# Performance work log

Hardware: AMD Instinct MI355X
Metric: run time of the kernel (lower is better)

## Reference

```python
import jax, jax.numpy as jnp
import numpy as np


def _gru(x, h, Wih, Whh, bih, bhh):
    # torch.nn.GRUCell math. x:(1,in), h:(1,H), Wih:(3H,in), Whh:(3H,H)
    gi = x @ Wih.T + bih
    gh = h @ Whh.T + bhh
    i_r, i_z, i_n = jnp.split(gi, 3, axis=-1)
    h_r, h_z, h_n = jnp.split(gh, 3, axis=-1)
    r = jax.nn.sigmoid(i_r + h_r)
    z = jax.nn.sigmoid(i_z + h_z)
    n = jnp.tanh(i_n + r * h_n)
    return (1.0 - z) * n + z * h


def _combine(S, Wa, ba, va):
    # SelfAttention.combine: additive attention over the stack axis.
    # S:(k,1,H), Wa:(H,A), ba:(A,), va:(A,)
    e = jnp.tanh(S @ Wa + ba) @ va          # (k,1) energies
    w = jax.nn.softmax(e, axis=0)            # softmax over stacked hidden states
    return jnp.sum(w[..., None] * S, axis=0)  # (1,H)


def setup_inputs() -> dict:
    key = jax.random.key(0)
    ks = jax.random.split(key, 20)
    T, F, H, A, L = 16384, 2048, 16, 64, 6
    G = 3 * H
    s = 0.1  # weight scale for numerical sanity
    return {
        "batch": jax.random.normal(ks[0], (T, 1, F), jnp.float32),
        "h0": jax.random.normal(ks[1], (L, 1, H), jnp.float32),
        "W_ih0": jax.random.normal(ks[2], (G, F), jnp.float32) * s,
        "W_hh0": jax.random.normal(ks[3], (G, H), jnp.float32) * s,
        "b_ih0": jax.random.normal(ks[4], (G,), jnp.float32) * s,
        "b_hh0": jax.random.normal(ks[5], (G,), jnp.float32) * s,
        "W_ih": jax.random.normal(ks[6], (L - 1, G, H), jnp.float32) * s,
        "W_hh": jax.random.normal(ks[7], (L - 1, G, H), jnp.float32) * s,
        "b_ih": jax.random.normal(ks[8], (L - 1, G), jnp.float32) * s,
        "b_hh": jax.random.normal(ks[9], (L - 1, G), jnp.float32) * s,
        "Wa": jax.random.normal(ks[10], (L, H, A), jnp.float32) * s,
        "ba": jax.random.normal(ks[11], (L, A), jnp.float32) * s,
        "va": jax.random.normal(ks[12], (L, A), jnp.float32) * s,
        "fc1_w": jax.random.normal(ks[13], (32, H), jnp.float32) * s,
        "fc1_b": jax.random.normal(ks[14], (32,), jnp.float32) * s,
        "fc2_w": jax.random.normal(ks[15], (1, 32), jnp.float32) * s,
        "fc2_b": jax.random.normal(ks[16], (1,), jnp.float32) * s,
    }


def reference(batch, h0, W_ih0, W_hh0, b_ih0, b_hh0, W_ih, W_hh, b_ih, b_hh,
              Wa, ba, va, fc1_w, fc1_b, fc2_w, fc2_b):
    L = Wa.shape[0]

    def step(h_s, x):
        # h_s: (L,1,H) carried hidden states, x: (1,F) current token
        inp = x.reshape(1, -1)
        new = []
        for l in range(L):
            if l == 0:
                inp = _gru(inp, h_s[0], W_ih0, W_hh0, b_ih0, b_hh0)
            else:
                inp = _gru(inp, h_s[l], W_ih[l - 1], W_hh[l - 1], b_ih[l - 1], b_hh[l - 1])
            new.append(inp)
        newS = jnp.stack(new)  # (L,1,H)
        # layer i attends over hidden states of layers i..L-1 (feedback combine)
        h_next = jnp.stack([_combine(newS[i:], Wa[i], ba[i], va[i]) for i in range(L)])
        top = h_next[-1].reshape(-1)  # (H,); dropout is identity in eval mode
        out = (top @ fc1_w.T + fc1_b) @ fc2_w.T + fc2_b  # (1,)
        return h_next, out

    _, outs = jax.lax.scan(step, h0, batch)
    return outs  # (T,1)
```

## Files before the change

### kernel.cpp

```cpp
#include <hip/hip_runtime.h>
#include <cstdint>
#include <cstddef>


#define TT 16384
#define FF 2048
#define HH 16
#define LL 6
#define GG 48
#define CHUNK 64
#define LOG2E 1.44269504088896340736f

__device__ float g_gi0p[(TT + CHUNK) * 64];

__device__ __forceinline__ float exp2_(float x) { return __builtin_amdgcn_exp2f(x); }
__device__ __forceinline__ float rcp_(float x) { return __builtin_amdgcn_rcpf(x); }
__device__ __forceinline__ float sig_n(float s) { return rcp_(1.f + exp2_(s)); }
__device__ __forceinline__ float tanh_p(float s) { return fmaf(-2.f, rcp_(exp2_(s) + 1.f), 1.f); }

#define MEMBAR() __asm__ __volatile__("" ::: "memory")

__device__ __forceinline__ float rdlane(float v, int l) {
  union { float f; int i; } a, b;
  a.f = v; b.i = __builtin_amdgcn_readlane(a.i, l); return b.f;
}
template <int CTRL>
__device__ __forceinline__ float dppf(float v) {
  union { float f; int i; } a, b;
  a.f = v; b.i = __builtin_amdgcn_mov_dpp(a.i, CTRL, 0xF, 0xF, true); return b.f;
}
template <int Q>
__device__ __forceinline__ float qbcast(float v) { return dppf<Q | (Q << 2) | (Q << 4) | (Q << 6)>(v); }

__device__ __forceinline__ float rowsum16(float v) {
  v += dppf<0xB1>(v);
  v += dppf<0x4E>(v);
  v += dppf<0x141>(v);
  v += dppf<0x140>(v);
  return v;
}
__device__ __forceinline__ float dot16r(const float (&w)[16], const float (&h)[16]) {
  float s0 = w[0] * h[0], s1 = w[1] * h[1], s2 = w[2] * h[2], s3 = w[3] * h[3];
#pragma unroll
  for (int k = 4; k < 16; k += 4) {
    s0 = fmaf(w[k], h[k], s0);       s1 = fmaf(w[k + 1], h[k + 1], s1);
    s2 = fmaf(w[k + 2], h[k + 2], s2); s3 = fmaf(w[k + 3], h[k + 3], s3);
  }
  return (s0 + s1) + (s2 + s3);
}
__device__ __forceinline__ float dot16i(const float (&w)[16], const float (&h)[16], float init) {
  float s0 = fmaf(w[0], h[0], init), s1 = w[1] * h[1], s2 = w[2] * h[2], s3 = w[3] * h[3];
#pragma unroll
  for (int k = 4; k < 16; k += 4) {
    s0 = fmaf(w[k], h[k], s0);       s1 = fmaf(w[k + 1], h[k + 1], s1);
    s2 = fmaf(w[k + 2], h[k + 2], s2); s3 = fmaf(w[k + 3], h[k + 3], s3);
  }
  return (s0 + s1) + (s2 + s3);
}

__device__ __forceinline__ int ldAcq(int* f) {
  return __hip_atomic_load(f, __ATOMIC_ACQUIRE, __HIP_MEMORY_SCOPE_WORKGROUP);
}
__device__ __forceinline__ void pollGE(int* f, int target) {
  while (ldAcq(f) < target) {}
}
__device__ __forceinline__ void waitFlag(int* f, int& cache, int need) {
  if (cache < need) { do { cache = ldAcq(f); } while (cache < need); }
}
__device__ __forceinline__ void sigRel(int* f, int v) {
  __hip_atomic_store(f, v, __ATOMIC_RELAXED, __HIP_MEMORY_SCOPE_WORKGROUP);
}

__device__ __forceinline__ void combBlock(const float4 A0, const float4 A1, const float4 A2,
                                          const float4 A3, float nsv,
                                          const float (&Wa)[16], float ba, float va,
                                          const float (&Wh)[16],
                                          float& S, float& ha, float& Pa) {
  float nr[16] = {A0.x, A0.y, A0.z, A0.w, A1.x, A1.y, A1.z, A1.w,
                  A2.x, A2.y, A2.z, A2.w, A3.x, A3.y, A3.z, A3.w};
  float u = dot16i(Wa, nr, ba);
  float P = dot16r(Wh, nr);
  float pe = va * tanh_p(u);
  float r = rowsum16(pe);
  float e = (rdlane(r, 0) + rdlane(r, 16)) + (rdlane(r, 32) + rdlane(r, 48));
  float w = exp2_(e);
  S += w; ha = fmaf(w, nsv, ha); Pa = fmaf(w, P, Pa);
}

__global__ __launch_bounds__(256) void gi0_gemm(const float* __restrict__ X,
                                                const float* __restrict__ W,
                                                const float* __restrict__ bias) {
  __shared__ float xs[64][132];
  __shared__ float ws[48][132];
  const int tid = threadIdx.x;
  const int t0 = blockIdx.x * 64;
  const int tg = tid & 15;
  const int tt = tid >> 4;
  float acc[4][3];
#pragma unroll
  for (int u = 0; u < 4; ++u)
#pragma unroll
    for (int v = 0; v < 3; ++v) acc[u][v] = 0.f;

  for (int k0 = 0; k0 < FF; k0 += 128) {
#pragma unroll
    for (int i = 0; i < 32; ++i) {
      int e = tid + 256 * i; int r = e >> 7, c = e & 127;
      xs[r][c] = X[(size_t)(t0 + r) * FF + k0 + c];
    }
#pragma unroll
    for (int i = 0; i < 24; ++i) {
      int e = tid + 256 * i; int r = e >> 7, c = e & 127;
      ws[r][c] = W[(size_t)r * FF + k0 + c];
    }
    __syncthreads();
#pragma unroll 8
    for (int c = 0; c < 128; ++c) {
      float x0 = xs[tt][c], x1 = xs[tt + 16][c], x2 = xs[tt + 32][c], x3 = xs[tt + 48][c];
      float w0 = ws[tg][c], w1 = ws[tg + 16][c], w2 = ws[tg + 32][c];
      acc[0][0] += x0 * w0; acc[0][1] += x0 * w1; acc[0][2] += x0 * w2;
      acc[1][0] += x1 * w0; acc[1][1] += x1 * w1; acc[1][2] += x1 * w2;
      acc[2][0] += x2 * w0; acc[2][1] += x2 * w1; acc[2][2] += x2 * w2;
      acc[3][0] += x3 * w0; acc[3][1] += x3 * w1; acc[3][2] += x3 * w2;
    }
    __syncthreads();
  }
  const float gsc3[3] = {-LOG2E, -LOG2E, 2.f * LOG2E};
#pragma unroll
  for (int u = 0; u < 4; ++u)
#pragma unroll
    for (int v = 0; v < 3; ++v)
      g_gi0p[(size_t)(t0 + tt + 16 * u) * 64 + tg * 4 + v] =
          (acc[u][v] + bias[tg + 16 * v]) * gsc3[v];
}

__global__ __launch_bounds__(512, 1) void fbrnn_scan(
    const float* __restrict__ h0,
    const float* __restrict__ Whh0, const float* __restrict__ bhh0,
    const float* __restrict__ Wih, const float* __restrict__ Whh,
    const float* __restrict__ bih, const float* __restrict__ bhh,
    const float* __restrict__ Wa, const float* __restrict__ ba,
    const float* __restrict__ va,
    const float* __restrict__ fc1w, const float* __restrict__ fc1b,
    const float* __restrict__ fc2w, const float* __restrict__ fc2b,
    float* __restrict__ out) {
  __shared__ __align__(16) float nsS[2][LL * HH];
  __shared__ __align__(16) float4 recS[5 * 64];
  __shared__ __align__(16) float4 partS[4 * 64];
  __shared__ __align__(16) float nsOut[256 * HH];
  __shared__ __align__(16) float chunkS[2][CHUNK * 64];
  __shared__ int flagNs;
  __shared__ int flagChunk;
  __shared__ int flagOut;
  __shared__ int gen5[2];

  const int tid = threadIdx.x;
  const int wv = tid >> 6;
  const int lane = tid & 63;
  const int qg = lane & 3;
  const int kk = lane >> 2;
  const int gate = (qg < 3 ? qg : 2);
  const int G = gate * 16 + kk;
  const float gsc = (gate == 2) ? 2.f * LOG2E : -LOG2E;

  const bool isChain = (wv == 0);
  const bool isStream = (wv == 4);
  const bool isFc = (wv == 6);
  const bool isIdle = (wv == 1);
  const int hRow = (wv == 6) ? 0 : (wv == 2) ? 1 : -1;
  const int pRow = (wv == 3) ? 2 : (wv == 7) ? 3 : (wv == 5) ? 4 : -1;
  const int pSlot = (wv == 6) ? 0 : (wv == 2) ? 2 : -1;

  float WBih[5][16];
  float WB5[16];  float bhh5R = 0.f;
  float Wa0R[16], Wh0R[16], Wa1R[16], Wh1R[16];
  float ba0R = 0.f, va0R = 0.f, bb0 = 0.f;
  float ba1R = 0.f, va1R = 0.f, bb1 = 0.f;
  float WaP[16], WhP[16];
  float baP = 0.f, vaP = 0.f, bhhP = 0.f;
  float WaH[16], WhH[16];
  float baH = 0.f, vaH = 0.f;
  float fc1R[16];
  float fb1 = 0.f, fw2 = 0.f, fb2 = 0.f;

  if (isChain) {
#pragma unroll
    for (int l = 0; l < 5; ++l)
#pragma unroll
      for (int k = 0; k < 16; ++k) WBih[l][k] = Wih[((l * GG) + G) * 16 + k] * gsc;
#pragma unroll
    for (int k = 0; k < 16; ++k) WB5[k] = Whh[(4 * GG + G) * 16 + k] * gsc;
    bhh5R = (bhh[4 * GG + G] + bih[4 * GG + G]) * gsc;
#pragma unroll
    for (int k = 0; k < 16; ++k) {
      Wa0R[k] = Wa[(0 * 16 + k) * 64 + lane] * (2.f * LOG2E);
      Wa1R[k] = Wa[(1 * 16 + k) * 64 + lane] * (2.f * LOG2E);
      Wh0R[k] = Whh0[G * 16 + k] * gsc;
      Wh1R[k] = Whh[(0 * GG + G) * 16 + k] * gsc;
    }
    ba0R = ba[0 * 64 + lane] * (2.f * LOG2E); va0R = va[0 * 64 + lane] * LOG2E;
    ba1R = ba[1 * 64 + lane] * (2.f * LOG2E); va1R = va[1 * 64 + lane] * LOG2E;
    bb0 = bhh0[G] * gsc;
    bb1 = (bhh[0 * GG + G] + bih[0 * GG + G]) * gsc;
  }
  if (pRow >= 0) {
#pragma unroll
    for (int k = 0; k < 16; ++k) WaP[k] = Wa[(pRow * 16 + k) * 64 + lane] * (2.f * LOG2E);
    baP = ba[pRow * 64 + lane] * (2.f * LOG2E);
    vaP = va[pRow * 64 + lane] * LOG2E;
    const float* ws = Whh + ((pRow - 1) * GG + G) * 16;
#pragma unroll
    for (int k = 0; k < 16; ++k) WhP[k] = ws[k] * gsc;
    bhhP = (bhh[(pRow - 1) * GG + G] + bih[(pRow - 1) * GG + G]) * gsc;
  }
  if (hRow >= 0) {
#pragma unroll
    for (int k = 0; k < 16; ++k) WaH[k] = Wa[(hRow * 16 + k) * 64 + lane] * (2.f * LOG2E);
    baH = ba[hRow * 64 + lane] * (2.f * LOG2E);
    vaH = va[hRow * 64 + lane] * LOG2E;
    const float* ws = (hRow == 0) ? (Whh0 + G * 16) : (Whh + ((hRow - 1) * GG + G) * 16);
#pragma unroll
    for (int k = 0; k < 16; ++k) WhH[k] = ws[k] * gsc;
  }
  if (isFc) {
    const int m = lane & 31;
#pragma unroll
    for (int k = 0; k < 16; ++k) fc1R[k] = fc1w[m * 16 + k];
    fb1 = fc1b[m]; fw2 = fc2w[m]; fb2 = fc2b[0];
  }

  if (tid == 0) { flagNs = 0; flagChunk = 1; flagOut = 0; gen5[0] = 0; gen5[1] = 0; }

  float hv5m = 0.f, gh5reg = 0.f;
  float gh0n = 0.f, hv0m = 0.f, gh1n = 0.f, hv1m = 0.f;
  if (isChain) {
    float hr[16];
#pragma unroll
    for (int k = 0; k < 16; ++k) hr[k] = h0[5 * 16 + k];
    hv5m = h0[5 * 16 + kk] - 1.f;
    gh5reg = dot16i(WB5, hr, bhh5R);
#pragma unroll
    for (int k = 0; k < 16; ++k) hr[k] = h0[0 * 16 + k];
    hv0m = h0[0 * 16 + kk] - 1.f;
    gh0n = dot16i(Wh0R, hr, bb0);
#pragma unroll
    for (int k = 0; k < 16; ++k) hr[k] = h0[1 * 16 + k];
    hv1m = h0[1 * 16 + kk] - 1.f;
    gh1n = dot16i(Wh1R, hr, bb1);
  } else if (pRow >= 0) {
    float hr[16];
#pragma unroll
    for (int k = 0; k < 16; ++k) hr[k] = h0[pRow * 16 + k];
    float4 rr;
    rr.x = dot16i(WhP, hr, bhhP);
    rr.y = h0[pRow * 16 + kk] - 1.f;
    rr.z = __int_as_float(0);
    rr.w = 0.f;
    recS[pRow * 64 + lane] = rr;
  }
  if (isStream) {
    const float4* src = (const float4*)g_gi0p;
    float4* dst = (float4*)(&chunkS[0][0]);
#pragma unroll
    for (int q = 0; q < 16; ++q) dst[q * 64 + lane] = src[q * 64 + lane];
  }
  if (pSlot >= 0) partS[pSlot * 64 + lane] = make_float4(0.f, 0.f, 0.f, __int_as_float(0));
  __syncthreads();

  if (isIdle) return;

#define EBLOCK(J, WaX, baX, vaX, WhX, Sx, hax, Pax) do {                          \
    waitFlag(&flagNs, fcache, t * 8 + (J) + 1);                                   \
    const float4* np_ = (const float4*)&nsS[nb][(J) * 16];                        \
    float4 A0_ = np_[0], A1_ = np_[1], A2_ = np_[2], A3_ = np_[3];                \
    float nsv_ = nsS[nb][(J) * 16 + kk];                                          \
    combBlock(A0_, A1_, A2_, A3_, nsv_, WaX, baX, vaX, WhX, Sx, hax, Pax);        \
  } while (0)

#define TAILFIN(ROW, Sv, hav, Pav) do {                                           \
    float4 A0, A1, A2, A3; float nsv5;                                            \
    for (;;) {                                                                    \
      int g5 = ldAcq(&gen5[nb]);                                                  \
      MEMBAR();                                                                   \
      const float4* np = (const float4*)&nsS[nb][5 * 16];                         \
      A0 = np[0]; A1 = np[1]; A2 = np[2]; A3 = np[3];                             \
      nsv5 = nsS[nb][5 * 16 + kk];                                                \
      MEMBAR();                                                                   \
      if (g5 >= tgt) break;                                                       \
    }                                                                             \
    combBlock(A0, A1, A2, A3, nsv5, WaP, baP, vaP, WhP, Sv, hav, Pav);            \
    const float inv_ = rcp_(Sv);                                                  \
    float4 rr_; rr_.x = fmaf(Pav, inv_, bhhP); rr_.y = fmaf(hav, inv_, -1.f);     \
    rr_.z = __int_as_float(tgt); rr_.w = 0.f;                                     \
    recS[(ROW) * 64 + lane] = rr_;                                                \
  } while (0)

  if (isStream) {
#pragma unroll 1
    for (int c = 1; c < 256; ++c) {
      if (c >= 2) pollGE(&flagNs, ((c - 1) * 64 - 1) * 8 + 1);
      const float4* src = (const float4*)(g_gi0p + ((size_t)c << 12));
      float4* dst = (float4*)(&chunkS[c & 1][0]);
#pragma unroll
      for (int q = 0; q < 16; ++q) dst[q * 64 + lane] = src[q * 64 + lane];
      MEMBAR();
      sigRel(&flagChunk, c + 1);
    }
    return;
  }

  if (isFc) {
    int fcache = 0;
#pragma unroll 1
    for (int t = 0; t < TT; ++t) {
      const int nb = t & 1;
      float Sh = 0.f, hah = 0.f, Pah = 0.f;
      EBLOCK(0, WaH, baH, vaH, WhH, Sh, hah, Pah);
      EBLOCK(1, WaH, baH, vaH, WhH, Sh, hah, Pah);
      EBLOCK(2, WaH, baH, vaH, WhH, Sh, hah, Pah);
      MEMBAR();
      partS[0 * 64 + lane] = make_float4(Sh, hah, Pah, __int_as_float(t + 1));
      MEMBAR();
      waitFlag(&flagNs, fcache, t * 8 + 6);
      const float4* np = (const float4*)(nsOut + (t & 255) * 16);
      float4 a0 = np[0], a1 = np[1], a2 = np[2], a3 = np[3];
      float nr[16] = {a0.x, a0.y, a0.z, a0.w, a1.x, a1.y, a1.z, a1.w,
                      a2.x, a2.y, a2.z, a2.w, a3.x, a3.y, a3.z, a3.w};
      float y = dot16i(fc1R, nr, fb1);
      float p = rowsum16(y * fw2);
      float o = rdlane(p, 0) + rdlane(p, 16) + fb2;
      if (lane == 0) out[t] = o;
      MEMBAR();
      sigRel(&flagOut, t + 1);
    }
    return;
  }

  if (!isChain) {
    int fcache = 0;
    if (wv == 2) {
#pragma unroll 1
      for (int t = 0; t < TT; ++t) {
        const int nb = t & 1;
        float Sh = 0.f, hah = 0.f, Pah = 0.f;
        EBLOCK(1, WaH, baH, vaH, WhH, Sh, hah, Pah);
        EBLOCK(2, WaH, baH, vaH, WhH, Sh, hah, Pah);
        MEMBAR();
        partS[2 * 64 + lane] = make_float4(Sh, hah, Pah, __int_as_float(t + 1));
        MEMBAR();
      }
    } else if (wv == 3) {
#pragma unroll 1
      for (int t = 0; t < TT; ++t) {
        const int nb = t & 1;
        const int tgt = t + 1;
        float S = 0.f, ha = 0.f, Pa = 0.f;
        EBLOCK(2, WaP, baP, vaP, WhP, S, ha, Pa);
        EBLOCK(3, WaP, baP, vaP, WhP, S, ha, Pa);
        EBLOCK(4, WaP, baP, vaP, WhP, S, ha, Pa);
        TAILFIN(2, S, ha, Pa);
      }
    } else if (wv == 7) {
#pragma unroll 1
      for (int t = 0; t < TT; ++t) {
        const int nb = t & 1;
        const int tgt = t + 1;
        float S = 0.f, ha = 0.f, Pa = 0.f;
        EBLOCK(3, WaP, baP, vaP, WhP, S, ha, Pa);
        EBLOCK(4, WaP, baP, vaP, WhP, S, ha, Pa);
        TAILFIN(3, S, ha, Pa);
      }
    } else {
#pragma unroll 1
      for (int t = 0; t < TT; ++t) {
        const int nb = t & 1;
        const int tgt = t + 1;
        float S = 0.f, ha = 0.f, Pa = 0.f;
        EBLOCK(4, WaP, baP, vaP, WhP, S, ha, Pa);
        TAILFIN(4, S, ha, Pa);
      }
    }
    return;
  }

  float gnext = chunkS[0][lane];
  float ns_sg[16];
#pragma unroll 1
  for (int t = 0; t < TT; ++t) {
    const int wb = t & 1;

    float ghv[6], hvm1[6];
    ghv[0] = gh0n; hvm1[0] = hv0m;
    ghv[1] = gh1n; hvm1[1] = hv1m;
    ghv[5] = gh5reg; hvm1[5] = hv5m;
    float4 r2, r3, r4;
    float gpre = 0.f;
    float gi0v = gnext;
    float ns = 0.f;
    float S0a = 0.f, ha0a = 0.f, Pa0a = 0.f;
    float S1a = 0.f, ha1a = 0.f, Pa1a = 0.f;
#pragma unroll
    for (int l = 0; l < 6; ++l) {
      if (l == 2) {
        if (!((__float_as_int(r2.z) >= t) & (__float_as_int(r3.z) >= t) &
              (__float_as_int(r4.z) >= t))) {
          do {
            MEMBAR();
            r2 = recS[2 * 64 + lane]; r3 = recS[3 * 64 + lane]; r4 = recS[4 * 64 + lane];
            MEMBAR();
          } while (!((__float_as_int(r2.z) >= t) & (__float_as_int(r3.z) >= t) &
                     (__float_as_int(r4.z) >= t)));
        }
        ghv[2] = r2.x; hvm1[2] = r2.y;
        ghv[3] = r3.x; hvm1[3] = r3.y;
        ghv[4] = r4.x; hvm1[4] = r4.y;
      }
      const float gh_g = ghv[l];
      const float s = (l == 0) ? (gi0v + gh_g) : dot16i(WBih[l - 1], ns_sg, gh_g);
      const float sg = sig_n(s);
      const float smg = s - gh_g;
      const float sr = qbcast<0>(sg);
      const float sz = qbcast<1>(sg);
      const float nb2 = fmaf(2.f, sz, -2.f);
      const float apb = fmaf(sz, hvm1[l], 1.f);
      const float E = exp2_(fmaf(sr, gh_g, smg));
      const float R = rcp_(E + 1.f);
      ns = fmaf(nb2, R, apb);
      if (qg == 2) {
        nsS[wb][l * 16 + kk] = ns;
        if (l == 5) nsOut[(t & 255) * 16 + kk] = ns;
      }
      MEMBAR();
      if (l == 5 && lane == 0) { sigRel(&gen5[wb], t + 1); sigRel(&flagNs, t * 8 + 6); }
#pragma unroll
      for (int k = 0; k < 16; ++k) ns_sg[k] = rdlane(ns, 4 * k + 2);
      if (l < 5 && lane == 0) sigRel(&flagNs, t * 8 + l + 1);
      if (l == 0) {
        if ((t & 63) == 63) {
          const int cn = (t + 1) >> 6;
          if (cn < 256) pollGE(&flagChunk, cn + 1);
        }
        if ((t & 63) == 32) pollGE(&flagOut, t - 64);
        gpre = chunkS[((t + 1) >> 6) & 1][((t + 1) & 63) * 64 + lane];
        MEMBAR();
        r2 = recS[2 * 64 + lane]; r3 = recS[3 * 64 + lane]; r4 = recS[4 * 64 + lane];
        MEMBAR();
      }
      if (l == 3 || l == 4) {
        const float nsq = qbcast<2>(ns);
        float uj0 = dot16i(Wa0R, ns_sg, ba0R);
        float uj1 = dot16i(Wa1R, ns_sg, ba1R);
        float Pj0 = dot16r(Wh0R, ns_sg);
        float Pj1 = dot16r(Wh1R, ns_sg);
        float pj0 = va0R * tanh_p(uj0);
        float pj1 = va1R * tanh_p(uj1);
        float rj0 = rowsum16(pj0);
        float rj1 = rowsum16(pj1);
        float ej0 = (rdlane(rj0, 0) + rdlane(rj0, 16)) + (rdlane(rj0, 32) + rdlane(rj0, 48));
        float ej1 = (rdlane(rj1, 0) + rdlane(rj1, 16)) + (rdlane(rj1, 32) + rdlane(rj1, 48));
        float wj0_ = exp2_(ej0), wj1_ = exp2_(ej1);
        S0a += wj0_; ha0a = fmaf(wj0_, nsq, ha0a); Pa0a = fmaf(wj0_, Pj0, Pa0a);
        S1a += wj1_; ha1a = fmaf(wj1_, nsq, ha1a); Pa1a = fmaf(wj1_, Pj1, Pa1a);
      }
    }
    MEMBAR();
    float4 q0 = partS[0 * 64 + lane], q2 = partS[2 * 64 + lane];
    MEMBAR();
    const float hv5n = qbcast<2>(ns);
    gh5reg = dot16i(WB5, ns_sg, bhh5R);
    float u0 = dot16i(Wa0R, ns_sg, ba0R);
    float u1 = dot16i(Wa1R, ns_sg, ba1R);
    float P0 = dot16r(Wh0R, ns_sg);
    float P1 = dot16r(Wh1R, ns_sg);
    float pe0 = va0R * tanh_p(u0);
    float pe1 = va1R * tanh_p(u1);
    float rs0 = rowsum16(pe0);
    float rs1 = rowsum16(pe1);
    float e0 = (rdlane(rs0, 0) + rdlane(rs0, 16)) + (rdlane(rs0, 32) + rdlane(rs0, 48));
    float e1 = (rdlane(rs1, 0) + rdlane(rs1, 16)) + (rdlane(rs1, 32) + rdlane(rs1, 48));
    float wj0 = exp2_(e0), wj1 = exp2_(e1);
    const int tp = t + 1;
    if (!((__float_as_int(q0.w) >= tp) & (__float_as_int(q2.w) >= tp))) {
      do {
        MEMBAR();
        q0 = partS[0 * 64 + lane]; q2 = partS[2 * 64 + lane];
        MEMBAR();
      } while (!((__float_as_int(q0.w) >= tp) & (__float_as_int(q2.w) >= tp)));
    }
    float S0 = q0.x + S0a + wj0;
    float hT0 = q0.y + ha0a + wj0 * hv5n;
    float PT0 = q0.z + Pa0a + wj0 * P0;
    float S1 = q2.x + S1a + wj1;
    float hT1 = q2.y + ha1a + wj1 * hv5n;
    float PT1 = q2.z + Pa1a + wj1 * P1;
    const float inv0 = rcp_(S0);
    const float inv1 = rcp_(S1);
    gh0n = fmaf(PT0, inv0, bb0); hv0m = fmaf(hT0, inv0, -1.f);
    gh1n = fmaf(PT1, inv1, bb1); hv1m = fmaf(hT1, inv1, -1.f);
    hv5m = hv5n - 1.f;
    gnext = gpre;
  }
}

extern "C" void kernel_launch(void* const* d_in, const int* in_sizes, int n_in,
                              void* d_out, int out_size, void* d_ws, size_t ws_size,
                              hipStream_t stream) {
  const float* batch = (const float*)d_in[0];
  const float* h0    = (const float*)d_in[1];
  const float* Wih0  = (const float*)d_in[2];
  const float* Whh0  = (const float*)d_in[3];
  const float* bih0  = (const float*)d_in[4];
  const float* bhh0  = (const float*)d_in[5];
  const float* Wih   = (const float*)d_in[6];
  const float* Whh   = (const float*)d_in[7];
  const float* bih   = (const float*)d_in[8];
  const float* bhh   = (const float*)d_in[9];
  const float* Wa    = (const float*)d_in[10];
  const float* ba    = (const float*)d_in[11];
  const float* va    = (const float*)d_in[12];
  const float* fc1w  = (const float*)d_in[13];
  const float* fc1b  = (const float*)d_in[14];
  const float* fc2w  = (const float*)d_in[15];
  const float* fc2b  = (const float*)d_in[16];
  float* out = (float*)d_out;
  (void)in_sizes; (void)n_in; (void)out_size; (void)d_ws; (void)ws_size;

  gi0_gemm<<<TT / 64, 256, 0, stream>>>(batch, Wih0, bih0);
  fbrnn_scan<<<1, 512, 0, stream>>>(h0, Whh0, bhh0, Wih, Whh, bih, bhh,
                                    Wa, ba, va, fc1w, fc1b, fc2w, fc2b, out);
}
```

Baseline: 27.54 ms.

## Offload layer 0/1/5 attention finalisation from chain wave to dedicated wavefronts

The chain wavefront no longer computes the attention combine for rows 0 and 1 or the layer-5 recurrent projection. Those move to the previously idle wave 1, which waits on the layer-5 state and gathers six partial sums from other waves. Partial-sum work is redistributed across waves 2, 3, 5, 6 and 7, and results are published through recS slots that the chain polls. This shortens the serial critical path per step, at the cost of an extra cross-wave handoff through shared memory that the chain must wait on before layer 0.

```diff
diff --git a/kernel.cpp b/kernel.cpp
--- a/kernel.cpp
+++ b/kernel.cpp
@@ -145,8 +145,8 @@
     const float* __restrict__ fc2w, const float* __restrict__ fc2b,
     float* __restrict__ out) {
   __shared__ __align__(16) float nsS[2][LL * HH];
-  __shared__ __align__(16) float4 recS[5 * 64];
-  __shared__ __align__(16) float4 partS[4 * 64];
+  __shared__ __align__(16) float4 recS[6 * 64];
+  __shared__ __align__(16) float4 partS[6 * 64];
   __shared__ __align__(16) float nsOut[256 * HH];
   __shared__ __align__(16) float chunkS[2][CHUNK * 64];
   __shared__ int flagNs;
@@ -164,99 +164,95 @@
   const float gsc = (gate == 2) ? 2.f * LOG2E : -LOG2E;
 
   const bool isChain = (wv == 0);
+  const bool isFin = (wv == 1);
   const bool isStream = (wv == 4);
   const bool isFc = (wv == 6);
-  const bool isIdle = (wv == 1);
-  const int hRow = (wv == 6) ? 0 : (wv == 2) ? 1 : -1;
-  const int pRow = (wv == 3) ? 2 : (wv == 7) ? 3 : (wv == 5) ? 4 : -1;
-  const int pSlot = (wv == 6) ? 0 : (wv == 2) ? 2 : -1;
+  const int tailRow = (wv == 3) ? 2 : (wv == 7) ? 3 : (wv == 5) ? 4 : -1;
 
   float WBih[5][16];
   float WB5[16];  float bhh5R = 0.f;
   float Wa0R[16], Wh0R[16], Wa1R[16], Wh1R[16];
   float ba0R = 0.f, va0R = 0.f, bb0 = 0.f;
   float ba1R = 0.f, va1R = 0.f, bb1 = 0.f;
-  float WaP[16], WhP[16];
-  float baP = 0.f, vaP = 0.f, bhhP = 0.f;
-  float WaH[16], WhH[16];
-  float baH = 0.f, vaH = 0.f;
-  float fc1R[16];
-  float fb1 = 0.f, fw2 = 0.f, fb2 = 0.f;
+  float WaA[16], WhA[16]; float baA = 0.f, vaA = 0.f;
+  float WaB[16], WhB[16]; float baB = 0.f, vaB = 0.f;
+  float WaT[16], WhT[16]; float baT = 0.f, vaT = 0.f, bhT = 0.f;
+  float fc1R[16]; float fb1 = 0.f, fw2 = 0.f, fb2 = 0.f;
+
+#define LOADROW(R, WaX, baX, vaX, WhX) do {                                      \
+    _Pragma("unroll") for (int k = 0; k < 16; ++k)                               \
+      WaX[k] = Wa[((R) * 16 + k) * 64 + lane] * (2.f * LOG2E);                   \
+    baX = ba[(R) * 64 + lane] * (2.f * LOG2E);                                   \
+    vaX = va[(R) * 64 + lane] * LOG2E;                                           \
+    { const float* ws_ = ((R) == 0) ? (Whh0 + G * 16)                            \
+                                    : (Whh + (((R) - 1) * GG + G) * 16);         \
+      _Pragma("unroll") for (int k = 0; k < 16; ++k) WhX[k] = ws_[k] * gsc; }    \
+  } while (0)
+#define LOADBH(R, bhX) do {                                                      \
+    bhX = (((R) == 0) ? bhh0[G]                                                  \
+                      : (bhh[((R) - 1) * GG + G] + bih[((R) - 1) * GG + G])) *   \
+          gsc;                                                                   \
+  } while (0)
 
   if (isChain) {
 #pragma unroll
     for (int l = 0; l < 5; ++l)
 #pragma unroll
       for (int k = 0; k < 16; ++k) WBih[l][k] = Wih[((l * GG) + G) * 16 + k] * gsc;
+  } else if (isFin) {
 #pragma unroll
     for (int k = 0; k < 16; ++k) WB5[k] = Whh[(4 * GG + G) * 16 + k] * gsc;
     bhh5R = (bhh[4 * GG + G] + bih[4 * GG + G]) * gsc;
-#pragma unroll
-    for (int k = 0; k < 16; ++k) {
-      Wa0R[k] = Wa[(0 * 16 + k) * 64 + lane] * (2.f * LOG2E);
-      Wa1R[k] = Wa[(1 * 16 + k) * 64 + lane] * (2.f * LOG2E);
-      Wh0R[k] = Whh0[G * 16 + k] * gsc;
-      Wh1R[k] = Whh[(0 * GG + G) * 16 + k] * gsc;
-    }
-    ba0R = ba[0 * 64 + lane] * (2.f * LOG2E); va0R = va[0 * 64 + lane] * LOG2E;
-    ba1R = ba[1 * 64 + lane] * (2.f * LOG2E); va1R = va[1 * 64 + lane] * LOG2E;
-    bb0 = bhh0[G] * gsc;
-    bb1 = (bhh[0 * GG + G] + bih[0 * GG + G]) * gsc;
-  }
-  if (pRow >= 0) {
-#pragma unroll
-    for (int k = 0; k < 16; ++k) WaP[k] = Wa[(pRow * 16 + k) * 64 + lane] * (2.f * LOG2E);
-    baP = ba[pRow * 64 + lane] * (2.f * LOG2E);
-    vaP = va[pRow * 64 + lane] * LOG2E;
-    const float* ws = Whh + ((pRow - 1) * GG + G) * 16;
-#pragma unroll
-    for (int k = 0; k < 16; ++k) WhP[k] = ws[k] * gsc;
-    bhhP = (bhh[(pRow - 1) * GG + G] + bih[(pRow - 1) * GG + G]) * gsc;
-  }
-  if (hRow >= 0) {
-#pragma unroll
-    for (int k = 0; k < 16; ++k) WaH[k] = Wa[(hRow * 16 + k) * 64 + lane] * (2.f * LOG2E);
-    baH = ba[hRow * 64 + lane] * (2.f * LOG2E);
-    vaH = va[hRow * 64 + lane] * LOG2E;
-    const float* ws = (hRow == 0) ? (Whh0 + G * 16) : (Whh + ((hRow - 1) * GG + G) * 16);
-#pragma unroll
-    for (int k = 0; k < 16; ++k) WhH[k] = ws[k] * gsc;
-  }
-  if (isFc) {
+    LOADROW(0, Wa0R, ba0R, va0R, Wh0R); LOADBH(0, bb0);
+    LOADROW(1, Wa1R, ba1R, va1R, Wh1R); LOADBH(1, bb1);
+  } else if (isFc) {
+    LOADROW(0, WaA, baA, vaA, WhA);
     const int m = lane & 31;
 #pragma unroll
     for (int k = 0; k < 16; ++k) fc1R[k] = fc1w[m * 16 + k];
     fb1 = fc1b[m]; fw2 = fc2w[m]; fb2 = fc2b[0];
+  } else if (wv == 2) {
+    LOADROW(1, WaA, baA, vaA, WhA);
+    LOADROW(0, WaB, baB, vaB, WhB);
+  } else if (wv == 3) {
+    LOADROW(2, WaT, baT, vaT, WhT); LOADBH(2, bhT);
+  } else if (wv == 5) {
+    LOADROW(1, WaA, baA, vaA, WhA);
+    LOADROW(4, WaT, baT, vaT, WhT); LOADBH(4, bhT);
+  } else if (wv == 7) {
+    LOADROW(1, WaA, baA, vaA, WhA);
+    LOADROW(3, WaT, baT, vaT, WhT); LOADBH(3, bhT);
   }
 
   if (tid == 0) { flagNs = 0; flagChunk = 1; flagOut = 0; gen5[0] = 0; gen5[1] = 0; }
 
-  float hv5m = 0.f, gh5reg = 0.f;
-  float gh0n = 0.f, hv0m = 0.f, gh1n = 0.f, hv1m = 0.f;
-  if (isChain) {
+  if (isFin) {
     float hr[16];
 #pragma unroll
+    for (int k = 0; k < 16; ++k) hr[k] = h0[0 * 16 + k];
+    float4 r0i; r0i.x = dot16i(Wh0R, hr, bb0); r0i.y = h0[0 * 16 + kk] - 1.f;
+    r0i.z = __int_as_float(0); r0i.w = 0.f;
+    recS[0 * 64 + lane] = r0i;
+#pragma unroll
+    for (int k = 0; k < 16; ++k) hr[k] = h0[1 * 16 + k];
+    float4 r1i; r1i.x = dot16i(Wh1R, hr, bb1); r1i.y = h0[1 * 16 + kk] - 1.f;
+    r1i.z = __int_as_float(0); r1i.w = 0.f;
+    recS[1 * 64 + lane] = r1i;
+#pragma unroll
     for (int k = 0; k < 16; ++k) hr[k] = h0[5 * 16 + k];
-    hv5m = h0[5 * 16 + kk] - 1.f;
-    gh5reg = dot16i(WB5, hr, bhh5R);
-#pragma unroll
-    for (int k = 0; k < 16; ++k) hr[k] = h0[0 * 16 + k];
-    hv0m = h0[0 * 16 + kk] - 1.f;
-    gh0n = dot16i(Wh0R, hr, bb0);
-#pragma unroll
-    for (int k = 0; k < 16; ++k) hr[k] = h0[1 * 16 + k];
-    hv1m = h0[1 * 16 + kk] - 1.f;
-    gh1n = dot16i(Wh1R, hr, bb1);
-  } else if (pRow >= 0) {
+    float4 r5i; r5i.x = dot16i(WB5, hr, bhh5R); r5i.y = h0[5 * 16 + kk] - 1.f;
+    r5i.z = __int_as_float(0); r5i.w = 0.f;
+    recS[5 * 64 + lane] = r5i;
+  } else if (tailRow >= 0) {
     float hr[16];
 #pragma unroll
-    for (int k = 0; k < 16; ++k) hr[k] = h0[pRow * 16 + k];
+    for (int k = 0; k < 16; ++k) hr[k] = h0[tailRow * 16 + k];
     float4 rr;
-    rr.x = dot16i(WhP, hr, bhhP);
-    rr.y = h0[pRow * 16 + kk] - 1.f;
+    rr.x = dot16i(WhT, hr, bhT);
+    rr.y = h0[tailRow * 16 + kk] - 1.f;
     rr.z = __int_as_float(0);
     rr.w = 0.f;
-    recS[pRow * 64 + lane] = rr;
+    recS[tailRow * 64 + lane] = rr;
   }
   if (isStream) {
     const float4* src = (const float4*)g_gi0p;
@@ -264,10 +260,12 @@
 #pragma unroll
     for (int q = 0; q < 16; ++q) dst[q * 64 + lane] = src[q * 64 + lane];
   }
-  if (pSlot >= 0) partS[pSlot * 64 + lane] = make_float4(0.f, 0.f, 0.f, __int_as_float(0));
+  if (isFc) {
+#pragma unroll
+    for (int s = 0; s < 6; ++s)
+      partS[s * 64 + lane] = make_float4(0.f, 0.f, 0.f, __int_as_float(0));
+  }
   __syncthreads();
-
-  if (isIdle) return;
 
 #define EBLOCK(J, WaX, baX, vaX, WhX, Sx, hax, Pax) do {                          \
     waitFlag(&flagNs, fcache, t * 8 + (J) + 1);                                   \
@@ -275,6 +273,12 @@
     float4 A0_ = np_[0], A1_ = np_[1], A2_ = np_[2], A3_ = np_[3];                \
     float nsv_ = nsS[nb][(J) * 16 + kk];                                          \
     combBlock(A0_, A1_, A2_, A3_, nsv_, WaX, baX, vaX, WhX, Sx, hax, Pax);        \
+  } while (0)
+
+#define POSTP(SLOT, Sx, hax, Pax) do {                                            \
+    MEMBAR();                                                                     \
+    partS[(SLOT) * 64 + lane] = make_float4(Sx, hax, Pax, __int_as_float(t + 1)); \
+    MEMBAR();                                                                     \
   } while (0)
 
 #define TAILFIN(ROW, Sv, hav, Pav) do {                                           \
@@ -288,9 +292,9 @@
       MEMBAR();                                                                   \
       if (g5 >= tgt) break;                                                       \
     }                                                                             \
-    combBlock(A0, A1, A2, A3, nsv5, WaP, baP, vaP, WhP, Sv, hav, Pav);            \
+    combBlock(A0, A1, A2, A3, nsv5, WaT, baT, vaT, WhT, Sv, hav, Pav);            \
     const float inv_ = rcp_(Sv);                                                  \
-    float4 rr_; rr_.x = fmaf(Pav, inv_, bhhP); rr_.y = fmaf(hav, inv_, -1.f);     \
+    float4 rr_; rr_.x = fmaf(Pav, inv_, bhT); rr_.y = fmaf(hav, inv_, -1.f);      \
     rr_.z = __int_as_float(tgt); rr_.w = 0.f;                                     \
     recS[(ROW) * 64 + lane] = rr_;                                                \
   } while (0)
@@ -309,24 +313,88 @@
     return;
   }
 
+  if (isFin) {
+#pragma unroll 1
+    for (int t = 0; t < TT; ++t) {
+      const int nb = t & 1;
+      const int tgt = t + 1;
+      float4 A0, A1, A2, A3; float nsv5;
+      for (;;) {
+        int g5 = ldAcq(&gen5[nb]);
+        MEMBAR();
+        const float4* np = (const float4*)&nsS[nb][5 * 16];
+        A0 = np[0]; A1 = np[1]; A2 = np[2]; A3 = np[3];
+        nsv5 = nsS[nb][5 * 16 + kk];
+        MEMBAR();
+        if (g5 >= tgt) break;
+      }
+      float nr[16] = {A0.x, A0.y, A0.z, A0.w, A1.x, A1.y, A1.z, A1.w,
+                      A2.x, A2.y, A2.z, A2.w, A3.x, A3.y, A3.z, A3.w};
+      float u0 = dot16i(Wa0R, nr, ba0R);
+      float u1 = dot16i(Wa1R, nr, ba1R);
+      float P0 = dot16r(Wh0R, nr);
+      float P1 = dot16r(Wh1R, nr);
+      float g5d = dot16i(WB5, nr, bhh5R);
+      float pe0 = va0R * tanh_p(u0);
+      float pe1 = va1R * tanh_p(u1);
+      float rs0 = rowsum16(pe0);
+      float rs1 = rowsum16(pe1);
+      float e0 = (rdlane(rs0, 0) + rdlane(rs0, 16)) + (rdlane(rs0, 32) + rdlane(rs0, 48));
+      float e1 = (rdlane(rs1, 0) + rdlane(rs1, 16)) + (rdlane(rs1, 32) + rdlane(rs1, 48));
+      float wj0 = exp2_(e0), wj1 = exp2_(e1);
+      float4 q0, q1, q2, q3, q4, q5;
+      for (;;) {
+        MEMBAR();
+        q0 = partS[0 * 64 + lane]; q1 = partS[1 * 64 + lane]; q2 = partS[2 * 64 + lane];
+        q3 = partS[3 * 64 + lane]; q4 = partS[4 * 64 + lane]; q5 = partS[5 * 64 + lane];
+        MEMBAR();
+        int ok = (__float_as_int(q0.w) >= tgt) & (__float_as_int(q1.w) >= tgt) &
+                 (__float_as_int(q2.w) >= tgt) & (__float_as_int(q3.w) >= tgt) &
+                 (__float_as_int(q4.w) >= tgt) & (__float_as_int(q5.w) >= tgt);
+        if (ok) break;
+      }
+      float S0 = q0.x + q1.x + q2.x + wj0;
+      float hT0 = q0.y + q1.y + q2.y + wj0 * nsv5;
+      float PT0 = q0.z + q1.z + q2.z + wj0 * P0;
+      float S1 = q3.x + q4.x + q5.x + wj1;
+      float hT1 = q3.y + q4.y + q5.y + wj1 * nsv5;
+      float PT1 = q3.z + q4.z + q5.z + wj1 * P1;
+      const float inv0 = rcp_(S0);
+      const float inv1 = rcp_(S1);
+      float4 w0r; w0r.x = fmaf(PT0, inv0, bb0); w0r.y = fmaf(hT0, inv0, -1.f);
+      w0r.z = __int_as_float(tgt); w0r.w = 0.f;
+      float4 w1r; w1r.x = fmaf(PT1, inv1, bb1); w1r.y = fmaf(hT1, inv1, -1.f);
+      w1r.z = __int_as_float(tgt); w1r.w = 0.f;
+      float4 w5r; w5r.x = g5d; w5r.y = nsv5 - 1.f;
+      w5r.z = __int_as_float(tgt); w5r.w = 0.f;
+      MEMBAR();
+      recS[0 * 64 + lane] = w0r;
+      recS[1 * 64 + lane] = w1r;
+      recS[5 * 64 + lane] = w5r;
+      MEMBAR();
+    }
+    return;
+  }
+
   if (isFc) {
     int fcache = 0;
 #pragma unroll 1
     for (int t = 0; t < TT; ++t) {
       const int nb = t & 1;
-      float Sh = 0.f, hah = 0.f, Pah = 0.f;
-      EBLOCK(0, WaH, baH, vaH, WhH, Sh, hah, Pah);
-      EBLOCK(1, WaH, baH, vaH, WhH, Sh, hah, Pah);
-      EBLOCK(2, WaH, baH, vaH, WhH, Sh, hah, Pah);
-      MEMBAR();
-      partS[0 * 64 + lane] = make_float4(Sh, hah, Pah, __int_as_float(t + 1));
-      MEMBAR();
+      float S = 0.f, ha = 0.f, Pa = 0.f;
+      EBLOCK(0, WaA, baA, vaA, WhA, S, ha, Pa);
+      EBLOCK(1, WaA, baA, vaA, WhA, S, ha, Pa);
+      EBLOCK(2, WaA, baA, vaA, WhA, S, ha, Pa);
+      POSTP(0, S, ha, Pa);
+      S = 0.f; ha = 0.f; Pa = 0.f;
+      EBLOCK(4, WaA, baA, vaA, WhA, S, ha, Pa);
+      POSTP(2, S, ha, Pa);
       waitFlag(&flagNs, fcache, t * 8 + 6);
       const float4* np = (const float4*)(nsOut + (t & 255) * 16);
       float4 a0 = np[0], a1 = np[1], a2 = np[2], a3 = np[3];
-      float nr[16] = {a0.x, a0.y, a0.z, a0.w, a1.x, a1.y, a1.z, a1.w,
-                      a2.x, a2.y, a2.z, a2.w, a3.x, a3.y, a3.z, a3.w};
-      float y = dot16i(fc1R, nr, fb1);
+      float nrf[16] = {a0.x, a0.y, a0.z, a0.w, a1.x, a1.y, a1.z, a1.w,
+                       a2.x, a2.y, a2.z, a2.w, a3.x, a3.y, a3.z, a3.w};
+      float y = dot16i(fc1R, nrf, fb1);
       float p = rowsum16(y * fw2);
       float o = rdlane(p, 0) + rdlane(p, 16) + fb2;
       if (lane == 0) out[t] = o;
@@ -342,23 +410,25 @@
 #pragma unroll 1
       for (int t = 0; t < TT; ++t) {
         const int nb = t & 1;
-        float Sh = 0.f, hah = 0.f, Pah = 0.f;
-        EBLOCK(1, WaH, baH, vaH, WhH, Sh, hah, Pah);
-        EBLOCK(2, WaH, baH, vaH, WhH, Sh, hah, Pah);
-        MEMBAR();
-        partS[2 * 64 + lane] = make_float4(Sh, hah, Pah, __int_as_float(t + 1));
-        MEMBAR();
-      }
-    } else if (wv == 3) {
+        float S = 0.f, ha = 0.f, Pa = 0.f;
+        EBLOCK(1, WaA, baA, vaA, WhA, S, ha, Pa);
+        EBLOCK(2, WaA, baA, vaA, WhA, S, ha, Pa);
+        POSTP(3, S, ha, Pa);
+        S = 0.f; ha = 0.f; Pa = 0.f;
+        EBLOCK(3, WaB, baB, vaB, WhB, S, ha, Pa);
+        POSTP(1, S, ha, Pa);
+      }
+    } else if (wv == 5) {
 #pragma unroll 1
       for (int t = 0; t < TT; ++t) {
         const int nb = t & 1;
         const int tgt = t + 1;
         float S = 0.f, ha = 0.f, Pa = 0.f;
-        EBLOCK(2, WaP, baP, vaP, WhP, S, ha, Pa);
-        EBLOCK(3, WaP, baP, vaP, WhP, S, ha, Pa);
-        EBLOCK(4, WaP, baP, vaP, WhP, S, ha, Pa);
-        TAILFIN(2, S, ha, Pa);
+        EBLOCK(3, WaA, baA, vaA, WhA, S, ha, Pa);
+        POSTP(4, S, ha, Pa);
+        S = 0.f; ha = 0.f; Pa = 0.f;
+        EBLOCK(4, WaT, baT, vaT, WhT, S, ha, Pa);
+        TAILFIN(4, S, ha, Pa);
       }
     } else if (wv == 7) {
 #pragma unroll 1
@@ -366,8 +436,11 @@
         const int nb = t & 1;
         const int tgt = t + 1;
         float S = 0.f, ha = 0.f, Pa = 0.f;
-        EBLOCK(3, WaP, baP, vaP, WhP, S, ha, Pa);
-        EBLOCK(4, WaP, baP, vaP, WhP, S, ha, Pa);
+        EBLOCK(3, WaT, baT, vaT, WhT, S, ha, Pa);
+        float Sb = 0.f, hab = 0.f, Pab = 0.f;
+        EBLOCK(4, WaA, baA, vaA, WhA, Sb, hab, Pab);
+        POSTP(5, Sb, hab, Pab);
+        EBLOCK(4, WaT, baT, vaT, WhT, S, ha, Pa);
         TAILFIN(3, S, ha, Pa);
       }
     } else {
@@ -376,8 +449,10 @@
         const int nb = t & 1;
         const int tgt = t + 1;
         float S = 0.f, ha = 0.f, Pa = 0.f;
-        EBLOCK(4, WaP, baP, vaP, WhP, S, ha, Pa);
-        TAILFIN(4, S, ha, Pa);
+        EBLOCK(2, WaT, baT, vaT, WhT, S, ha, Pa);
+        EBLOCK(3, WaT, baT, vaT, WhT, S, ha, Pa);
+        EBLOCK(4, WaT, baT, vaT, WhT, S, ha, Pa);
+        TAILFIN(2, S, ha, Pa);
       }
     }
     return;
@@ -389,31 +464,43 @@
   for (int t = 0; t < TT; ++t) {
     const int wb = t & 1;
 
+    if ((t & 63) == 63) {
+      const int cn = (t + 1) >> 6;
+      if (cn < 256) pollGE(&flagChunk, cn + 1);
+    }
+    if ((t & 63) == 32) pollGE(&flagOut, t - 64);
+    const float gpre = chunkS[((t + 1) >> 6) & 1][((t + 1) & 63) * 64 + lane];
+
+    float4 r0, r1;
+    for (;;) {
+      MEMBAR();
+      r0 = recS[0 * 64 + lane]; r1 = recS[1 * 64 + lane];
+      MEMBAR();
+      if ((__float_as_int(r0.z) >= t) & (__float_as_int(r1.z) >= t)) break;
+    }
     float ghv[6], hvm1[6];
-    ghv[0] = gh0n; hvm1[0] = hv0m;
-    ghv[1] = gh1n; hvm1[1] = hv1m;
-    ghv[5] = gh5reg; hvm1[5] = hv5m;
-    float4 r2, r3, r4;
-    float gpre = 0.f;
+    ghv[0] = r0.x; hvm1[0] = r0.y;
+    ghv[1] = r1.x; hvm1[1] = r1.y;
+    float4 r2, r3, r4, r5;
     float gi0v = gnext;
     float ns = 0.f;
-    float S0a = 0.f, ha0a = 0.f, Pa0a = 0.f;
-    float S1a = 0.f, ha1a = 0.f, Pa1a = 0.f;
 #pragma unroll
     for (int l = 0; l < 6; ++l) {
       if (l == 2) {
         if (!((__float_as_int(r2.z) >= t) & (__float_as_int(r3.z) >= t) &
-              (__float_as_int(r4.z) >= t))) {
+              (__float_as_int(r4.z) >= t) & (__float_as_int(r5.z) >= t))) {
           do {
             MEMBAR();
-            r2 = recS[2 * 64 + lane]; r3 = recS[3 * 64 + lane]; r4 = recS[4 * 64 + lane];
+            r2 = recS[2 * 64 + lane]; r3 = recS[3 * 64 + lane];
+            r4 = recS[4 * 64 + lane]; r5 = recS[5 * 64 + lane];
             MEMBAR();
           } while (!((__float_as_int(r2.z) >= t) & (__float_as_int(r3.z) >= t) &
-                     (__float_as_int(r4.z) >= t)));
+                     (__float_as_int(r4.z) >= t) & (__float_as_int(r5.z) >= t)));
         }
         ghv[2] = r2.x; hvm1[2] = r2.y;
         ghv[3] = r3.x; hvm1[3] = r3.y;
         ghv[4] = r4.x; hvm1[4] = r4.y;
+        ghv[5] = r5.x; hvm1[5] = r5.y;
       }
       const float gh_g = ghv[l];
       const float s = (l == 0) ? (gi0v + gh_g) : dot16i(WBih[l - 1], ns_sg, gh_g);
@@ -431,73 +518,20 @@
         if (l == 5) nsOut[(t & 255) * 16 + kk] = ns;
       }
       MEMBAR();
-      if (l == 5 && lane == 0) { sigRel(&gen5[wb], t + 1); sigRel(&flagNs, t * 8 + 6); }
-#pragma unroll
-      for (int k = 0; k < 16; ++k) ns_sg[k] = rdlane(ns, 4 * k + 2);
-      if (l < 5 && lane == 0) sigRel(&flagNs, t * 8 + l + 1);
+      if (l == 5) {
+        if (lane == 0) { sigRel(&gen5[wb], t + 1); sigRel(&flagNs, t * 8 + 6); }
+      } else {
+#pragma unroll
+        for (int k = 0; k < 16; ++k) ns_sg[k] = rdlane(ns, 4 * k + 2);
+        if (lane == 0) sigRel(&flagNs, t * 8 + l + 1);
+      }
       if (l == 0) {
-        if ((t & 63) == 63) {
-          const int cn = (t + 1) >> 6;
-          if (cn < 256) pollGE(&flagChunk, cn + 1);
-        }
-        if ((t & 63) == 32) pollGE(&flagOut, t - 64);
-        gpre = chunkS[((t + 1) >> 6) & 1][((t + 1) & 63) * 64 + lane];
         MEMBAR();
-        r2 = recS[2 * 64 + lane]; r3 = recS[3 * 64 + lane]; r4 = recS[4 * 64 + lane];
+        r2 = recS[2 * 64 + lane]; r3 = recS[3 * 64 + lane];
+        r4 = recS[4 * 64 + lane]; r5 = recS[5 * 64 + lane];
         MEMBAR();
       }
-      if (l == 3 || l == 4) {
-        const float nsq = qbcast<2>(ns);
-        float uj0 = dot16i(Wa0R, ns_sg, ba0R);
-        float uj1 = dot16i(Wa1R, ns_sg, ba1R);
-        float Pj0 = dot16r(Wh0R, ns_sg);
-        float Pj1 = dot16r(Wh1R, ns_sg);
-        float pj0 = va0R * tanh_p(uj0);
-        float pj1 = va1R * tanh_p(uj1);
-        float rj0 = rowsum16(pj0);
-        float rj1 = rowsum16(pj1);
-        float ej0 = (rdlane(rj0, 0) + rdlane(rj0, 16)) + (rdlane(rj0, 32) + rdlane(rj0, 48));
-        float ej1 = (rdlane(rj1, 0) + rdlane(rj1, 16)) + (rdlane(rj1, 32) + rdlane(rj1, 48));
-        float wj0_ = exp2_(ej0), wj1_ = exp2_(ej1);
-        S0a += wj0_; ha0a = fmaf(wj0_, nsq, ha0a); Pa0a = fmaf(wj0_, Pj0, Pa0a);
-        S1a += wj1_; ha1a = fmaf(wj1_, nsq, ha1a); Pa1a = fmaf(wj1_, Pj1, Pa1a);
-      }
-    }
-    MEMBAR();
-    float4 q0 = partS[0 * 64 + lane], q2 = partS[2 * 64 + lane];
-    MEMBAR();
-    const float hv5n = qbcast<2>(ns);
-    gh5reg = dot16i(WB5, ns_sg, bhh5R);
-    float u0 = dot16i(Wa0R, ns_sg, ba0R);
-    float u1 = dot16i(Wa1R, ns_sg, ba1R);
-    float P0 = dot16r(Wh0R, ns_sg);
-    float P1 = dot16r(Wh1R, ns_sg);
-    float pe0 = va0R * tanh_p(u0);
-    float pe1 = va1R * tanh_p(u1);
-    float rs0 = rowsum16(pe0);
-    float rs1 = rowsum16(pe1);
-    float e0 = (rdlane(rs0, 0) + rdlane(rs0, 16)) + (rdlane(rs0, 32) + rdlane(rs0, 48));
-    float e1 = (rdlane(rs1, 0) + rdlane(rs1, 16)) + (rdlane(rs1, 32) + rdlane(rs1, 48));
-    float wj0 = exp2_(e0), wj1 = exp2_(e1);
-    const int tp = t + 1;
-    if (!((__float_as_int(q0.w) >= tp) & (__float_as_int(q2.w) >= tp))) {
-      do {
-        MEMBAR();
-        q0 = partS[0 * 64 + lane]; q2 = partS[2 * 64 + lane];
-        MEMBAR();
-      } while (!((__float_as_int(q0.w) >= tp) & (__float_as_int(q2.w) >= tp)));
-    }
-    float S0 = q0.x + S0a + wj0;
-    float hT0 = q0.y + ha0a + wj0 * hv5n;
-    float PT0 = q0.z + Pa0a + wj0 * P0;
-    float S1 = q2.x + S1a + wj1;
-    float hT1 = q2.y + ha1a + wj1 * hv5n;
-    float PT1 = q2.z + Pa1a + wj1 * P1;
-    const float inv0 = rcp_(S0);
-    const float inv1 = rcp_(S1);
-    gh0n = fmaf(PT0, inv0, bb0); hv0m = fmaf(hT0, inv0, -1.f);
-    gh1n = fmaf(PT1, inv1, bb1); hv1m = fmaf(hT1, inv1, -1.f);
-    hv5m = hv5n - 1.f;
+    }
     gnext = gpre;
   }
 }
```

Result: no change. 27.45 ms (-0.3%).
